# Kernel tuning notes

Hardware: AMD Instinct MI355X
Metric: run time of the kernel (lower is better)

The kernel has to match this reference:

```python
import jax, jax.numpy as jnp
import numpy as np

N = 100_000   # nodes
E = 640_000   # edges
H = 128       # hidden_dim
L = 4         # num_layers
C = 2         # num_classes
G = 128       # graphs in batch

def setup_inputs() -> dict:
    key = jax.random.key(0)
    ks = jax.random.split(key, 8)
    x = jax.random.randint(ks[0], (N, 1), 0, 2)
    edge_index = jax.random.randint(ks[1], (2, E), 0, N)
    batch = jnp.sort(jax.random.randint(ks[2], (N,), 0, G))
    embed = jax.random.normal(ks[3], (2, H), jnp.float32)
    Ws = jax.random.normal(ks[4], (L, H, H), jnp.float32) * (1.0 / np.sqrt(H))
    bs = jnp.zeros((L, H), jnp.float32)
    W_out = jax.random.normal(ks[5], (H, C), jnp.float32) * (1.0 / np.sqrt(H))
    b_out = jnp.zeros((C,), jnp.float32)
    return dict(x=x, edge_index=edge_index, batch=batch, embed=embed,
                Ws=Ws, bs=bs, W_out=W_out, b_out=b_out)

def reference(x, edge_index, batch, embed, Ws, bs, W_out, b_out):
    src, dst = edge_index[0], edge_index[1]
    # symmetric GCN normalization with self-loops (PyG GCNConv default)
    deg = jax.ops.segment_sum(jnp.ones(E, jnp.float32), dst, num_segments=N) + 1.0
    dinv = jax.lax.rsqrt(deg)
    enorm = (dinv[src] * dinv[dst])[:, None]   # per-edge norm
    snorm = (dinv * dinv)[:, None]             # self-loop norm

    h = embed[x[:, 0]]                          # [N, H] embedding lookup
    n_layers = Ws.shape[0]
    for l in range(n_layers):
        t = h @ Ws[l]                           # linear transform [N, H]
        agg = jax.ops.segment_sum(t[src] * enorm, dst, num_segments=N) \
              + t * snorm + bs[l]
        h = jax.nn.relu(agg) if l < n_layers - 1 else agg

    # global mean pool over graph ids
    counts = jax.ops.segment_sum(jnp.ones(N, jnp.float32), batch, num_segments=G)
    pooled = jax.ops.segment_sum(h, batch, num_segments=G) \
             / jnp.maximum(counts, 1.0)[:, None]   # [G, H]
    return pooled @ W_out + b_out                  # [G, C]
```

## Files before the change

kernel.cpp:

```cpp
#include <hip/hip_runtime.h>

typedef __attribute__((ext_vector_type(8))) short bf16x8;
typedef __attribute__((ext_vector_type(4))) float f32x4;
typedef __attribute__((ext_vector_type(2))) float f32x2;

__device__ inline unsigned short bf16_rtn(float f) {
  unsigned u = __float_as_uint(f);
  unsigned r = u + 0x7fffu + ((u >> 16) & 1u);
  return (unsigned short)(r >> 16);
}

__device__ inline void split_bf16(float f, unsigned short& hi, unsigned short& lo) {
  hi = bf16_rtn(f);
  float fh = __uint_as_float((unsigned)hi << 16);
  lo = bf16_rtn(f - fh);
}

__device__ inline float bf16_to_f(unsigned short v) {
  return __uint_as_float((unsigned)v << 16);
}

__device__ inline unsigned char f_to_fp8(float f) {
  int r = __builtin_amdgcn_cvt_pk_fp8_f32(f, f, 0, false);
  return (unsigned char)(r & 0xff);
}
__device__ inline f32x2 fp8x2_to_f(unsigned short v) {
  return __builtin_amdgcn_cvt_pk_f32_fp8((int)v, false);
}


__global__ void k_hist(const int* __restrict__ dst, int* __restrict__ deg,
                       int* __restrict__ posr, int E) {
  int e = blockIdx.x * 256 + threadIdx.x;
  if (e < E) posr[e] = atomicAdd(&deg[dst[e]], 1);
}

__global__ void k_scan1(const int* __restrict__ deg, int* __restrict__ rowptr,
                        int* __restrict__ bsum, float* __restrict__ dpk,
                        const int* __restrict__ x, const int* __restrict__ batch,
                        int* __restrict__ gstart, int* __restrict__ gend, int N) {
  __shared__ int s[256];
  int t = threadIdx.x;
  int i = blockIdx.x * 256 + t;
  int v = (i < N) ? deg[i] : 0;
  if (i < N) {
    float di = rsqrtf((float)v + 1.0f);
    dpk[i] = x[i] ? -di : di;
    int g = batch[i];
    if (i == 0 || batch[i - 1] != g) gstart[g] = i;
    if (i == N - 1 || batch[i + 1] != g) gend[g] = i + 1;
  }
  s[t] = v;
  __syncthreads();
  for (int off = 1; off < 256; off <<= 1) {
    int u = (t >= off) ? s[t - off] : 0;
    __syncthreads();
    s[t] += u;
    __syncthreads();
  }
  if (i < N) rowptr[i] = s[t] - v;
  if (t == 255) bsum[blockIdx.x] = s[255];
}

__global__ void k_scan2(const int* __restrict__ bsum, int* __restrict__ boff, int nb) {
  __shared__ int s[512];
  int t = threadIdx.x;
  int v = (t < nb) ? bsum[t] : 0;
  s[t] = v;
  __syncthreads();
  for (int off = 1; off < 512; off <<= 1) {
    int u = (t >= off) ? s[t - off] : 0;
    __syncthreads();
    s[t] += u;
    __syncthreads();
  }
  boff[t] = s[t] - v;
}

__global__ void k_scan3(int* __restrict__ rowptr, const int* __restrict__ boff,
                        int N, int E) {
  int i = blockIdx.x * 256 + threadIdx.x;
  if (i < N) rowptr[i] += boff[i >> 8];
  if (i == 0) rowptr[N] = E;
}

__global__ void k_scatter(const int* __restrict__ src, const int* __restrict__ dst,
                          const int* __restrict__ posr, const int* __restrict__ rowptr,
                          const float* __restrict__ dpk,
                          int2* __restrict__ epack, int E) {
  int e = blockIdx.x * 256 + threadIdx.x;
  if (e >= E) return;
  int s = src[e], d = dst[e];
  int pos = rowptr[d] + posr[e];
  epack[pos] = make_int2(s, __float_as_int(dpk[s]));
}

__global__ void k_prepWT(const float* __restrict__ Ws, const float* __restrict__ embed,
                         unsigned short* __restrict__ wphi,
                         unsigned short* __restrict__ wplo,
                         float* __restrict__ T) {
  int l = blockIdx.x;
  if (l == 3) {
    int t = threadIdx.x;
    int r = t >> 7, c = t & 127;
    float acc = 0.f;
    for (int k = 0; k < 128; ++k)
      acc += embed[r * 128 + k] * Ws[k * 128 + c];
    T[r * 128 + c] = acc;
    return;
  }
  const float* W = Ws + (size_t)(l + 1) * 128 * 128;
  unsigned short* dh = wphi + (size_t)l * 16384;
  unsigned short* dl = wplo + (size_t)l * 16384;
  for (int idx = threadIdx.x; idx < 16384; idx += 256) {
    int j = idx & 7;
    int lane = (idx >> 3) & 63;
    int c = (idx >> 9) & 3;
    int ct = idx >> 11;
    int k = c * 32 + ((lane >> 4) * 8) + j;
    int n = ct * 16 + (lane & 15);
    unsigned short hi, lo;
    split_bf16(W[k * 128 + n], hi, lo);
    dh[idx] = hi;
    dl[idx] = lo;
  }
}

__device__ inline void gather_node(const unsigned char* __restrict__ tin,
                                   const int2* __restrict__ epack,
                                   int r0, int deg, int lane,
                                   float& a0, float& a1) {
  int dcap = deg < 64 ? deg : 64;
  int sl = 0;
  if (lane < dcap) sl = epack[r0 + lane].x;
  a0 = 0.f; a1 = 0.f;
  int e = 0;
  for (; e + 4 <= dcap; e += 4) {
    int s0 = __shfl(sl, e, 64),     s1 = __shfl(sl, e + 1, 64);
    int s2 = __shfl(sl, e + 2, 64), s3 = __shfl(sl, e + 3, 64);
    unsigned short p0 = *(const unsigned short*)(tin + (size_t)s0 * 128 + 2 * lane);
    unsigned short p1 = *(const unsigned short*)(tin + (size_t)s1 * 128 + 2 * lane);
    unsigned short p2 = *(const unsigned short*)(tin + (size_t)s2 * 128 + 2 * lane);
    unsigned short p3 = *(const unsigned short*)(tin + (size_t)s3 * 128 + 2 * lane);
    f32x2 v0 = fp8x2_to_f(p0), v1 = fp8x2_to_f(p1);
    f32x2 v2 = fp8x2_to_f(p2), v3 = fp8x2_to_f(p3);
    a0 += v0.x + v1.x + v2.x + v3.x;
    a1 += v0.y + v1.y + v2.y + v3.y;
  }
  for (; e < dcap; ++e) {
    int s = __shfl(sl, e, 64);
    unsigned short p = *(const unsigned short*)(tin + (size_t)s * 128 + 2 * lane);
    f32x2 v = fp8x2_to_f(p);
    a0 += v.x;
    a1 += v.y;
  }
  for (int ee = r0 + 64; ee < r0 + deg; ++ee) {
    int s = epack[ee].x;
    unsigned short p = *(const unsigned short*)(tin + (size_t)s * 128 + 2 * lane);
    f32x2 v = fp8x2_to_f(p);
    a0 += v.x;
    a1 += v.y;
  }
}

__global__ void k_agg(const unsigned char* __restrict__ tin,
                      const int* __restrict__ rowptr,
                      const int2* __restrict__ epack,
                      const float* __restrict__ dpk, const float* __restrict__ bvec,
                      unsigned short* __restrict__ h, int N, int dorelu) {
  int i = (blockIdx.x * blockDim.x + threadIdx.x) >> 6;
  int lane = threadIdx.x & 63;
  if (i >= N) return;
  int r0 = rowptr[i], r1 = rowptr[i + 1];
  float a0, a1;
  gather_node(tin, epack, r0, r1 - r0, lane, a0, a1);
  unsigned short ps = *(const unsigned short*)(tin + (size_t)i * 128 + 2 * lane);
  f32x2 sv = fp8x2_to_f(ps);
  float di = fabsf(dpk[i]);
  float2 bv = *(const float2*)(bvec + 2 * lane);
  a0 = di * (a0 + sv.x) + bv.x;
  a1 = di * (a1 + sv.y) + bv.y;
  if (dorelu) { a0 = fmaxf(a0, 0.f); a1 = fmaxf(a1, 0.f); }
  *(unsigned*)(h + (size_t)i * 128 + 2 * lane) =
      (unsigned)bf16_rtn(a0) | ((unsigned)bf16_rtn(a1) << 16);
}

__global__ void k_gemm(const unsigned short* __restrict__ h,
                       const unsigned short* __restrict__ wphi,
                       const unsigned short* __restrict__ wplo,
                       const float* __restrict__ dpk,
                       unsigned char* __restrict__ tout, int N) {
  int wave = threadIdx.x >> 6;
  int lane = threadIdx.x & 63;
  int r0 = (blockIdx.x * 4 + wave) * 32;
  if (r0 >= N) return;
  int q = lane >> 4;
  int m = lane & 15;
  const bf16x8* bh_base = (const bf16x8*)wphi;
  const bf16x8* bl_base = (const bf16x8*)wplo;

  f32x4 acc[2][8];
  #pragma unroll
  for (int tt = 0; tt < 2; ++tt)
    #pragma unroll
    for (int ct = 0; ct < 8; ++ct)
      acc[tt][ct] = (f32x4){0.f, 0.f, 0.f, 0.f};

  for (int c = 0; c < 4; ++c) {
    bf16x8 a0 = *(const bf16x8*)(h + (size_t)(r0 + m) * 128 + c * 32 + q * 8);
    bf16x8 a1 = *(const bf16x8*)(h + (size_t)(r0 + 16 + m) * 128 + c * 32 + q * 8);
    #pragma unroll
    for (int ct = 0; ct < 8; ++ct) {
      bf16x8 bh = bh_base[(ct * 4 + c) * 64 + lane];
      bf16x8 bl = bl_base[(ct * 4 + c) * 64 + lane];
      acc[0][ct] = __builtin_amdgcn_mfma_f32_16x16x32_bf16(a0, bh, acc[0][ct], 0, 0, 0);
      acc[0][ct] = __builtin_amdgcn_mfma_f32_16x16x32_bf16(a0, bl, acc[0][ct], 0, 0, 0);
      acc[1][ct] = __builtin_amdgcn_mfma_f32_16x16x32_bf16(a1, bh, acc[1][ct], 0, 0, 0);
      acc[1][ct] = __builtin_amdgcn_mfma_f32_16x16x32_bf16(a1, bl, acc[1][ct], 0, 0, 0);
    }
  }

  #pragma unroll
  for (int tt = 0; tt < 2; ++tt)
    #pragma unroll
    for (int ct = 0; ct < 8; ++ct)
      #pragma unroll
      for (int r = 0; r < 4; ++r) {
        int row = r0 + tt * 16 + q * 4 + r;
        if (row < N) {
          float sc = fabsf(dpk[row]);
          tout[(size_t)row * 128 + ct * 16 + m] = f_to_fp8(sc * acc[tt][ct][r]);
        }
      }
}

__global__ void k_pool_partial(const unsigned short* __restrict__ h,
                               const int* __restrict__ batch,
                               float* __restrict__ pooled, int N) {
  int c = threadIdx.x & 127;
  int half = threadIdx.x >> 7;
  int rbeg = blockIdx.x * 64 + half * 32;
  int rend = rbeg + 32;
  if (rend > N) rend = N;
  if (rbeg >= N) return;
  float acc = 0.f;
  int curg = batch[rbeg];
  for (int i = rbeg; i < rend; ++i) {
    int g = batch[i];
    if (g != curg) {
      atomicAdd(&pooled[curg * 128 + c], acc);
      acc = 0.f;
      curg = g;
    }
    acc += bf16_to_f(h[(size_t)i * 128 + c]);
  }
  atomicAdd(&pooled[curg * 128 + c], acc);
}

__device__ inline void gemm_tile8(const unsigned short* hT,
                                  const unsigned short* __restrict__ wphi,
                                  const unsigned short* __restrict__ wplo,
                                  const float* __restrict__ dpk,
                                  unsigned char* __restrict__ tout, int i0, int N) {
  int ct = threadIdx.x >> 6;
  int lane = threadIdx.x & 63;
  int q = lane >> 4;
  int m = lane & 15;
  const bf16x8* bh_base = (const bf16x8*)wphi;
  const bf16x8* bl_base = (const bf16x8*)wplo;

  f32x4 acc0 = (f32x4){0.f, 0.f, 0.f, 0.f};
  f32x4 acc1 = (f32x4){0.f, 0.f, 0.f, 0.f};

  #pragma unroll
  for (int c = 0; c < 4; ++c) {
    bf16x8 a0 = *(const bf16x8*)(hT + (m) * 136 + c * 32 + q * 8);
    bf16x8 a1 = *(const bf16x8*)(hT + (16 + m) * 136 + c * 32 + q * 8);
    bf16x8 bh = bh_base[(ct * 4 + c) * 64 + lane];
    bf16x8 bl = bl_base[(ct * 4 + c) * 64 + lane];
    acc0 = __builtin_amdgcn_mfma_f32_16x16x32_bf16(a0, bh, acc0, 0, 0, 0);
    acc0 = __builtin_amdgcn_mfma_f32_16x16x32_bf16(a0, bl, acc0, 0, 0, 0);
    acc1 = __builtin_amdgcn_mfma_f32_16x16x32_bf16(a1, bh, acc1, 0, 0, 0);
    acc1 = __builtin_amdgcn_mfma_f32_16x16x32_bf16(a1, bl, acc1, 0, 0, 0);
  }

  #pragma unroll
  for (int r = 0; r < 4; ++r) {
    int row0 = i0 + q * 4 + r;
    int row1 = row0 + 16;
    if (row0 < N) {
      float sc = fabsf(dpk[row0]);
      tout[(size_t)row0 * 128 + ct * 16 + m] = f_to_fp8(sc * acc0[r]);
    }
    if (row1 < N) {
      float sc = fabsf(dpk[row1]);
      tout[(size_t)row1 * 128 + ct * 16 + m] = f_to_fp8(sc * acc1[r]);
    }
  }
}

__global__ __launch_bounds__(512)
void k_l1_gemm(const int* __restrict__ rowptr,
               const int2* __restrict__ epack,
               const float* __restrict__ dpk, const float* __restrict__ T,
               const float* __restrict__ b0,
               const unsigned short* __restrict__ wphi,
               const unsigned short* __restrict__ wplo,
               unsigned char* __restrict__ tout, int N) {
  __shared__ unsigned short hT[32 * 136];
  int wave = threadIdx.x >> 6;
  int lane = threadIdx.x & 63;
  int i0 = blockIdx.x * 32;

  for (int j = wave * 4; j < wave * 4 + 4; ++j) {
    int i = i0 + j;
    if (i >= N) break;
    int r0 = rowptr[i], r1 = rowptr[i + 1];
    float sabs = 0.f, sneg = 0.f;
    for (int e = r0 + lane; e < r1; e += 64) {
      float wv = __int_as_float(epack[e].y);
      float aw = fabsf(wv);
      sabs += aw;
      if (wv < 0.f) sneg += aw;
    }
    for (int mm = 32; mm >= 1; mm >>= 1) {
      sabs += __shfl_xor(sabs, mm, 64);
      sneg += __shfl_xor(sneg, mm, 64);
    }
    float dp = dpk[i];
    float di = fabsf(dp);
    float sn = di * di;
    float c1 = di * sneg;
    float c0 = di * (sabs - sneg);
    if (dp < 0.f) c1 += sn; else c0 += sn;
    float v0 = fmaxf(c0 * T[2 * lane]     + c1 * T[128 + 2 * lane]     + b0[2 * lane],     0.f);
    float v1 = fmaxf(c0 * T[2 * lane + 1] + c1 * T[128 + 2 * lane + 1] + b0[2 * lane + 1], 0.f);
    *(unsigned*)&hT[j * 136 + 2 * lane] = (unsigned)bf16_rtn(v0) | ((unsigned)bf16_rtn(v1) << 16);
  }
  __syncthreads();
  gemm_tile8(hT, wphi, wplo, dpk, tout, i0, N);
}

__global__ void k_out(const float* __restrict__ pooled, const int* __restrict__ gstart,
                      const int* __restrict__ gend, const float* __restrict__ W_out,
                      const float* __restrict__ b_out, float* __restrict__ out, int G) {
  __shared__ float sp[128];
  int g = blockIdx.x;
  int j = threadIdx.x;
  float cnt = (float)(gend[g] - gstart[g]);
  sp[j] = pooled[g * 128 + j] / fmaxf(cnt, 1.f);
  __syncthreads();
  if (j < 2) {
    float o = b_out[j];
    for (int k = 0; k < 128; ++k)
      o += sp[k] * W_out[k * 2 + j];
    out[g * 2 + j] = o;
  }
}

extern "C" void kernel_launch(void* const* d_in, const int* in_sizes, int n_in,
                              void* d_out, int out_size, void* d_ws, size_t ws_size,
                              hipStream_t stream) {
  const int*   x     = (const int*)d_in[0];
  const int*   ei    = (const int*)d_in[1];
  const int*   batch = (const int*)d_in[2];
  const float* embed = (const float*)d_in[3];
  const float* Ws    = (const float*)d_in[4];
  const float* bs    = (const float*)d_in[5];
  const float* W_out = (const float*)d_in[6];
  const float* b_out = (const float*)d_in[7];
  float* out = (float*)d_out;

  int N = in_sizes[2];
  int E = in_sizes[1] / 2;
  int G = out_size / 2;

  const int* src = ei;
  const int* dst = ei + E;

  char* w = (char*)d_ws;
  auto alloc = [&](size_t bytes) {
    char* p = w;
    w += (bytes + 255) & ~(size_t)255;
    return p;
  };
  int*   deg    = (int*)  alloc((size_t)N * 4);
  float* dpk    = (float*)alloc((size_t)N * 4);
  int*   rowptr = (int*)  alloc((size_t)(N + 1) * 4);
  int*   posr   = (int*)  alloc((size_t)E * 4);
  int*   bsum   = (int*)  alloc(512 * 4);
  int*   boff   = (int*)  alloc(512 * 4);
  int*   gstart = (int*)  alloc((size_t)G * 4);
  int*   gend   = (int*)  alloc((size_t)G * 4);
  float* pooled = (float*)alloc((size_t)G * 128 * 4);
  float* T      = (float*)alloc(256 * 4);
  unsigned short* wphi = (unsigned short*)alloc((size_t)3 * 16384 * 2);
  unsigned short* wplo = (unsigned short*)alloc((size_t)3 * 16384 * 2);
  int2*  epack  = (int2*) alloc((size_t)E * 8);
  unsigned short* h = (unsigned short*)alloc((size_t)N * 128 * 2);
  unsigned char* t_a = (unsigned char*)alloc((size_t)N * 128);
  unsigned char* t_b = (unsigned char*)alloc((size_t)N * 128);

  int nbN = (N + 255) / 256;
  int nbE = (E + 255) / 256;
  int ntile = (N + 31) / 32;
  int nwb = (N + 3) / 4;
  int ngemm = (N + 127) / 128;

  size_t gzero = (size_t)((char*)pooled - (char*)gstart) + (size_t)G * 128 * 4;
  hipMemsetAsync(deg, 0, (size_t)N * 4, stream);
  hipMemsetAsync(gstart, 0, gzero, stream);

  k_hist<<<nbE, 256, 0, stream>>>(dst, deg, posr, E);
  k_scan1<<<nbN, 256, 0, stream>>>(deg, rowptr, bsum, dpk, x, batch, gstart, gend, N);
  k_scan2<<<1, 512, 0, stream>>>(bsum, boff, nbN);
  k_scan3<<<nbN, 256, 0, stream>>>(rowptr, boff, N, E);
  k_scatter<<<nbE, 256, 0, stream>>>(src, dst, posr, rowptr, dpk, epack, E);
  k_prepWT<<<4, 256, 0, stream>>>(Ws, embed, wphi, wplo, T);

  k_l1_gemm<<<ntile, 512, 0, stream>>>(rowptr, epack, dpk, T, bs,
                                       wphi, wplo, t_a, N);
  k_agg<<<nwb, 256, 0, stream>>>(t_a, rowptr, epack, dpk, bs + 128, h, N, 1);
  k_gemm<<<ngemm, 256, 0, stream>>>(h, wphi + 16384, wplo + 16384, dpk, t_b, N);
  k_agg<<<nwb, 256, 0, stream>>>(t_b, rowptr, epack, dpk, bs + 256, h, N, 1);
  k_gemm<<<ngemm, 256, 0, stream>>>(h, wphi + 32768, wplo + 32768, dpk, t_a, N);
  k_agg<<<nwb, 256, 0, stream>>>(t_a, rowptr, epack, dpk, bs + 384, h, N, 0);
  k_pool_partial<<<(N + 63) / 64, 256, 0, stream>>>(h, batch, pooled, N);
  k_out<<<G, 128, 0, stream>>>(pooled, gstart, gend, W_out, b_out, out, G);
}
```

Before: 349.1 us.

## Fuse final aggregation with mean-pool and replace memsets with a zero kernel

The last-layer aggregation now reduces each block's four node rows through shared memory and atomically adds them into the per-graph pooled sums. This removes the separate pooling kernel and the write and reread of h. The two memsets are replaced by one zeroing kernel, and the relu flag is dropped from k_agg. In exchange, the fused kernel issues far more atomics, about 128 per block across roughly 25k blocks, where the old pooling kernel accumulated runs of 32 rows before each atomic, so atomic contention may rise.

```diff
diff --git a/kernel.cpp b/kernel.cpp
--- a/kernel.cpp
+++ b/kernel.cpp
@@ -26,6 +26,12 @@
 }
 __device__ inline f32x2 fp8x2_to_f(unsigned short v) {
   return __builtin_amdgcn_cvt_pk_f32_fp8((int)v, false);
+}
+
+__global__ void k_zero(int* __restrict__ deg, int* __restrict__ gpz, int N, int M) {
+  int i = blockIdx.x * 256 + threadIdx.x;
+  if (i < N) deg[i] = 0;
+  if (i < M) gpz[i] = 0;
 }
 
 
@@ -167,7 +173,7 @@
                       const int* __restrict__ rowptr,
                       const int2* __restrict__ epack,
                       const float* __restrict__ dpk, const float* __restrict__ bvec,
-                      unsigned short* __restrict__ h, int N, int dorelu) {
+                      unsigned short* __restrict__ h, int N) {
   int i = (blockIdx.x * blockDim.x + threadIdx.x) >> 6;
   int lane = threadIdx.x & 63;
   if (i >= N) return;
@@ -178,11 +184,55 @@
   f32x2 sv = fp8x2_to_f(ps);
   float di = fabsf(dpk[i]);
   float2 bv = *(const float2*)(bvec + 2 * lane);
-  a0 = di * (a0 + sv.x) + bv.x;
-  a1 = di * (a1 + sv.y) + bv.y;
-  if (dorelu) { a0 = fmaxf(a0, 0.f); a1 = fmaxf(a1, 0.f); }
+  a0 = fmaxf(di * (a0 + sv.x) + bv.x, 0.f);
+  a1 = fmaxf(di * (a1 + sv.y) + bv.y, 0.f);
   *(unsigned*)(h + (size_t)i * 128 + 2 * lane) =
       (unsigned)bf16_rtn(a0) | ((unsigned)bf16_rtn(a1) << 16);
+}
+
+__global__ void k_agg_pool(const unsigned char* __restrict__ tin,
+                           const int* __restrict__ rowptr,
+                           const int2* __restrict__ epack,
+                           const float* __restrict__ dpk, const float* __restrict__ bvec,
+                           const int* __restrict__ batch,
+                           float* __restrict__ pooled, int N) {
+  __shared__ float sh[4][128];
+  __shared__ int sg[4];
+  int wave = threadIdx.x >> 6;
+  int lane = threadIdx.x & 63;
+  int i = blockIdx.x * 4 + wave;
+  if (threadIdx.x < 4) sg[threadIdx.x] = -1;
+  __syncthreads();
+  if (i < N) {
+    int r0 = rowptr[i], r1 = rowptr[i + 1];
+    float a0, a1;
+    gather_node(tin, epack, r0, r1 - r0, lane, a0, a1);
+    unsigned short ps = *(const unsigned short*)(tin + (size_t)i * 128 + 2 * lane);
+    f32x2 sv = fp8x2_to_f(ps);
+    float di = fabsf(dpk[i]);
+    float2 bv = *(const float2*)(bvec + 2 * lane);
+    sh[wave][2 * lane]     = di * (a0 + sv.x) + bv.x;
+    sh[wave][2 * lane + 1] = di * (a1 + sv.y) + bv.y;
+    if (lane == 0) sg[wave] = batch[i];
+  }
+  __syncthreads();
+  if (threadIdx.x < 128) {
+    int c = threadIdx.x;
+    float acc = 0.f;
+    int cur = sg[0];
+    #pragma unroll
+    for (int w2 = 0; w2 < 4; ++w2) {
+      int gw = sg[w2];
+      if (gw < 0) break;
+      if (gw != cur) {
+        atomicAdd(&pooled[cur * 128 + c], acc);
+        acc = 0.f;
+        cur = gw;
+      }
+      acc += sh[w2][c];
+    }
+    atomicAdd(&pooled[cur * 128 + c], acc);
+  }
 }
 
 __global__ void k_gemm(const unsigned short* __restrict__ h,
@@ -232,29 +282,6 @@
           tout[(size_t)row * 128 + ct * 16 + m] = f_to_fp8(sc * acc[tt][ct][r]);
         }
       }
-}
-
-__global__ void k_pool_partial(const unsigned short* __restrict__ h,
-                               const int* __restrict__ batch,
-                               float* __restrict__ pooled, int N) {
-  int c = threadIdx.x & 127;
-  int half = threadIdx.x >> 7;
-  int rbeg = blockIdx.x * 64 + half * 32;
-  int rend = rbeg + 32;
-  if (rend > N) rend = N;
-  if (rbeg >= N) return;
-  float acc = 0.f;
-  int curg = batch[rbeg];
-  for (int i = rbeg; i < rend; ++i) {
-    int g = batch[i];
-    if (g != curg) {
-      atomicAdd(&pooled[curg * 128 + c], acc);
-      acc = 0.f;
-      curg = g;
-    }
-    acc += bf16_to_f(h[(size_t)i * 128 + c]);
-  }
-  atomicAdd(&pooled[curg * 128 + c], acc);
 }
 
 __device__ inline void gemm_tile8(const unsigned short* hT,
@@ -406,11 +433,9 @@
   int ntile = (N + 31) / 32;
   int nwb = (N + 3) / 4;
   int ngemm = (N + 127) / 128;
-
-  size_t gzero = (size_t)((char*)pooled - (char*)gstart) + (size_t)G * 128 * 4;
-  hipMemsetAsync(deg, 0, (size_t)N * 4, stream);
-  hipMemsetAsync(gstart, 0, gzero, stream);
-
+  int M = G * 130;
+
+  k_zero<<<nbN, 256, 0, stream>>>(deg, gstart, N, M);
   k_hist<<<nbE, 256, 0, stream>>>(dst, deg, posr, E);
   k_scan1<<<nbN, 256, 0, stream>>>(deg, rowptr, bsum, dpk, x, batch, gstart, gend, N);
   k_scan2<<<1, 512, 0, stream>>>(bsum, boff, nbN);
@@ -420,11 +445,11 @@
 
   k_l1_gemm<<<ntile, 512, 0, stream>>>(rowptr, epack, dpk, T, bs,
                                        wphi, wplo, t_a, N);
-  k_agg<<<nwb, 256, 0, stream>>>(t_a, rowptr, epack, dpk, bs + 128, h, N, 1);
+  k_agg<<<nwb, 256, 0, stream>>>(t_a, rowptr, epack, dpk, bs + 128, h, N);
   k_gemm<<<ngemm, 256, 0, stream>>>(h, wphi + 16384, wplo + 16384, dpk, t_b, N);
-  k_agg<<<nwb, 256, 0, stream>>>(t_b, rowptr, epack, dpk, bs + 256, h, N, 1);
+  k_agg<<<nwb, 256, 0, stream>>>(t_b, rowptr, epack, dpk, bs + 256, h, N);
   k_gemm<<<ngemm, 256, 0, stream>>>(h, wphi + 32768, wplo + 32768, dpk, t_a, N);
-  k_agg<<<nwb, 256, 0, stream>>>(t_a, rowptr, epack, dpk, bs + 384, h, N, 0);
-  k_pool_partial<<<(N + 63) / 64, 256, 0, stream>>>(h, batch, pooled, N);
+  k_agg_pool<<<nwb, 256, 0, stream>>>(t_a, rowptr, epack, dpk, bs + 384,
+                                      batch, pooled, N);
   k_out<<<G, 128, 0, stream>>>(pooled, gstart, gend, W_out, b_out, out, G);
 }
```

Result: no change. 344.2 us (-1.4%).
